# Performance work log

Measured on AMD Instinct MI355X. Metric: run time of the kernel, lower is better.

## Reference

```python
import jax, jax.numpy as jnp
import numpy as np


def setup_inputs() -> dict:
    key = jax.random.key(0)
    k_x, k_qkv, k_proj, k_bias = jax.random.split(key, 4)
    b, n, dim = 4, 8192, 512
    h, w = 8, 256
    x = jax.random.normal(k_x, (b, n, dim), dtype=jnp.float32)
    # Linear weights stored as [in, out] (transpose of torch's [out, in])
    Wqkv = jax.random.normal(k_qkv, (dim, 3 * dim), dtype=jnp.float32) * 0.02
    bqkv = jnp.zeros((3 * dim,), dtype=jnp.float32)
    Wproj = jax.random.normal(k_proj, (dim, dim), dtype=jnp.float32) * 0.02
    bproj = jnp.zeros((dim,), dtype=jnp.float32)
    # torch init is zeros; use small randn so the bias path is exercised
    attn_bias = jax.random.normal(k_bias, (h, w, w), dtype=jnp.float32) * 0.02
    return {"x": x, "Wqkv": Wqkv, "bqkv": bqkv, "Wproj": Wproj,
            "bproj": bproj, "attn_bias": attn_bias}


def reference(x, Wqkv, bqkv, Wproj, bproj, attn_bias):
    b, n, c = x.shape
    h, w, _ = attn_bias.shape
    d = c // h
    nw = n // w  # number of non-overlapping windows (n divisible by w)
    qkv = (x @ Wqkv + bqkv).reshape(b, n, 3, h, d)
    q, k, v = jnp.moveaxis(qkv, 2, 0)  # each [b, n, h, d]

    def to_windows(t):
        # [b, n, h, d] -> [b, h, nw, w, d]
        return t.reshape(b, nw, w, h, d).transpose(0, 3, 1, 2, 4)

    q, k, v = to_windows(q), to_windows(k), to_windows(v)
    scale = d ** -0.5
    # block-local attention: [b, h, nw, w, w]
    attn = jnp.einsum('bhnqd,bhnkd->bhnqk', q, k) * scale + attn_bias[None, :, None]
    attn = jax.nn.softmax(attn, axis=-1)
    out = jnp.einsum('bhnqk,bhnkd->bhnqd', attn, v)
    # [b, h, nw, w, d] -> [b, n, h*d]
    out = out.transpose(0, 2, 3, 1, 4).reshape(b, n, c)
    return out @ Wproj + bproj
```

## Files before the change

### kernel.cpp

```cpp
#include <hip/hip_runtime.h>

typedef unsigned short u16;
typedef unsigned int u32;
typedef __bf16 bf16x8 __attribute__((ext_vector_type(8)));
typedef float f32x4 __attribute__((ext_vector_type(4)));


__device__ __forceinline__ u16 f2bf(float f) {
  u32 u = __builtin_bit_cast(u32, f);
  u32 r = (u + 0x7fffu + ((u >> 16) & 1u)) >> 16;
  return (u16)r;
}
__device__ __forceinline__ u32 pk2(float a, float b) {
  return (u32)f2bf(a) | ((u32)f2bf(b) << 16);
}
__device__ __forceinline__ f32x4 mfma16(bf16x8 a, bf16x8 b, f32x4 c) {
  return __builtin_amdgcn_mfma_f32_16x16x32_bf16(a, b, c, 0, 0, 0);
}
__device__ __forceinline__ void glds16(const void* g, void* l) {
  typedef __attribute__((address_space(1))) void as1_void;
  typedef __attribute__((address_space(3))) void as3_void;
  __builtin_amdgcn_global_load_lds((as1_void*)g, (as3_void*)l, 16, 0, 0);
}


__device__ __forceinline__ void transpose_body(const float* __restrict__ in,
                                               u16* __restrict__ out,
                                               int N, int n0, int k0) {
  __shared__ float t[32][33];
  int tx = threadIdx.x & 31, ty = threadIdx.x >> 5;
#pragma unroll
  for (int s = 0; s < 32; s += 8)
    t[ty + s][tx] = in[(long)(k0 + ty + s) * N + n0 + tx];
  __syncthreads();
#pragma unroll
  for (int s = 0; s < 32; s += 8)
    out[(long)(n0 + ty + s) * 512 + k0 + tx] = f2bf(t[tx][ty + s]);
}

__launch_bounds__(256)
__global__ void prep_k(const float* __restrict__ x, u16* __restrict__ xbf,
                       const float* __restrict__ Wqkv, u16* __restrict__ wqkvT,
                       const float* __restrict__ Wproj, u16* __restrict__ wprojT,
                       const float* __restrict__ bias, float* __restrict__ biasT) {
  const int id = blockIdx.x;
  if (id < 8192) {
    long i = ((long)id * 256 + threadIdx.x) * 8;
    float4 f0 = *(const float4*)(x + i);
    float4 f1 = *(const float4*)(x + i + 4);
    uint4 o;
    o.x = pk2(f0.x, f0.y);
    o.y = pk2(f0.z, f0.w);
    o.z = pk2(f1.x, f1.y);
    o.w = pk2(f1.z, f1.w);
    *(uint4*)(xbf + i) = o;
  } else if (id < 8960) {
    int bx = id - 8192;
    transpose_body(Wqkv, wqkvT, 1536, (bx % 48) * 32, (bx / 48) * 32);
  } else if (id < 9216) {
    int bx = id - 8960;
    transpose_body(Wproj, wprojT, 512, (bx & 15) * 32, (bx >> 4) * 32);
  } else {
    int hb = id - 9216;
    int h = hb >> 4, rt = hb & 15;
    int lane = threadIdx.x & 63;
    int quad = lane >> 4, l15 = lane & 15;
    int jtg = threadIdx.x >> 6;
    const float L = 1.44269504f;
#pragma unroll
    for (int i = 0; i < 4; ++i) {
      int jt = jtg * 4 + i;
      float4 v = *(const float4*)&bias[((long)h * 256 + rt * 16 + l15) * 256 + jt * 16 + quad * 4];
      v.x *= L; v.y *= L; v.z *= L; v.w *= L;
      *(float4*)&biasT[(((long)hb * 16 + jt) * 64 + lane) * 4] = v;
    }
  }
}


template <int EPI>
__device__ __forceinline__ void gemm_body(const u16* __restrict__ A, const u16* __restrict__ Bt,
                                          const float* __restrict__ bias,
                                          u16* __restrict__ oqk, u16* __restrict__ ovt,
                                          float* __restrict__ ofp,
                                          long arow0, long brow0) {
  constexpr int K = 512;
  __shared__ u16 Asm[8192];
  __shared__ u16 Bsm[8192];

  const int tid = threadIdx.x;
  const int wave = tid >> 6, lane = tid & 63;
  const int quad = lane >> 4, l15 = lane & 15;
  const int wm = wave >> 1, wn = wave & 1;
  const int gsw = quad ^ ((l15 >> 1) & 3);

  f32x4 acc[4][4] = {};

  for (int k0 = 0; k0 < K; k0 += 64) {
#pragma unroll
    for (int rd = 0; rd < 4; ++rd) {
      int flat = rd * 256 + tid;
      int c = flat >> 9, row = (flat >> 2) & 127, gp = flat & 3;
      int g = gp ^ ((row >> 1) & 3);
      const long koff = k0 + c * 32 + g * 8;
      glds16(A + (arow0 + row) * K + koff, &Asm[(rd * 256 + wave * 64) * 8]);
      glds16(Bt + (brow0 + row) * K + koff, &Bsm[(rd * 256 + wave * 64) * 8]);
    }
    __syncthreads();
#pragma unroll
    for (int c = 0; c < 2; ++c) {
      bf16x8 af[4], bfr[4];
#pragma unroll
      for (int i = 0; i < 4; ++i)
        af[i] = *(const bf16x8*)&Asm[c * 4096 + (wm * 64 + i * 16 + l15) * 32 + gsw * 8];
#pragma unroll
      for (int j = 0; j < 4; ++j)
        bfr[j] = *(const bf16x8*)&Bsm[c * 4096 + (wn * 64 + j * 16 + l15) * 32 + gsw * 8];
#pragma unroll
      for (int i = 0; i < 4; ++i)
#pragma unroll
        for (int j = 0; j < 4; ++j)
          acc[i][j] = mfma16(af[i], bfr[j], acc[i][j]);
    }
    __syncthreads();
  }

#pragma unroll
  for (int j = 0; j < 4; ++j) {
    const int C = (int)brow0 + wn * 64 + j * 16 + l15;
    const float bc = bias[C];
#pragma unroll
    for (int i = 0; i < 4; ++i) {
      const long R0 = arow0 + wm * 64 + i * 16 + quad * 4;
      float v4[4];
#pragma unroll
      for (int r = 0; r < 4; ++r) v4[r] = acc[i][j][r] + bc;
      if constexpr (EPI == 0) {
        if (C < 1024) {
#pragma unroll
          for (int r = 0; r < 4; ++r) oqk[(R0 + r) * 1024 + C] = f2bf(v4[r]);
        } else {
          const int hc = (C >> 6) & 7, dc = C & 63;
          const int b = (int)(R0 >> 13), n0 = (int)(R0 & 8191);
          uint2 w;
          w.x = pk2(v4[0], v4[1]);
          w.y = pk2(v4[2], v4[3]);
          *(uint2*)&ovt[((long)(b * 8 + hc) * 64 + dc) * 8192 + n0] = w;
        }
      } else {
#pragma unroll
        for (int r = 0; r < 4; ++r) ofp[(R0 + r) * 512 + C] = v4[r];
      }
    }
  }
}


__launch_bounds__(256)
__global__ void qkv_gemm_k(const u16* __restrict__ A, const u16* __restrict__ Bt,
                           const float* __restrict__ bias,
                           u16* __restrict__ oqk, u16* __restrict__ ovt) {
  int bid = blockIdx.x;
  int xcd = bid & 7, i = bid >> 3;
  int nt = i % 12, mtl = i / 12;
  gemm_body<0>(A, Bt, bias, oqk, ovt, nullptr,
               (long)(xcd * 32 + mtl) * 128, (long)nt * 128);
}

__launch_bounds__(256)
__global__ void proj_gemm_k(const u16* __restrict__ A, const u16* __restrict__ Bt,
                            const float* __restrict__ bias, float* __restrict__ ofp) {
  int bid = blockIdx.x;
  int xcd = bid & 7, i = bid >> 3;
  int nt = i & 3, mtl = i >> 2;
  gemm_body<1>(A, Bt, bias, nullptr, nullptr, ofp,
               (long)(xcd * 32 + mtl) * 128, (long)nt * 128);
}


__launch_bounds__(512, 4)
__global__ void attn_win(const u16* __restrict__ qk, const u16* __restrict__ vtb,
                         const float* __restrict__ biasT, u16* __restrict__ og) {
  __shared__ __align__(16) u16 kS[16384];
  __shared__ __align__(16) u16 vS[16384];
  __shared__ __align__(16) u16 pS[8][1024];

  const int tid = threadIdx.x;
  const int wave = tid >> 6, lane = tid & 63;
  const int quad = lane >> 4, l15 = lane & 15;
  const int gsw = quad ^ ((l15 >> 1) & 3);

  const int wi = blockIdx.x;
  const int xcd = wi & 7, hi = (wi >> 3) & 7, wl = wi >> 6;
  const int win = xcd * 16 + wl;
  const int nwi = win & 31, bi = win >> 5;
  const long grow = (long)bi * 8192 + nwi * 256;
  const u16* qp = qk + grow * 1024 + hi * 64;
  const u16* kp = qp + 512;
  const u16* vp = vtb + (long)(bi * 8 + hi) * 64 * 8192 + nwi * 256;

  bf16x8 bq[2][2];
#pragma unroll
  for (int sc = 0; sc < 2; ++sc) {
    const int q0 = wave * 32 + sc * 16;
    bq[sc][0] = *(const bf16x8*)&qp[(long)(q0 + l15) * 1024 + quad * 8];
    bq[sc][1] = *(const bf16x8*)&qp[(long)(q0 + l15) * 1024 + 32 + quad * 8];
  }

#pragma unroll
  for (int it = 0; it < 4; ++it) {
    int flat = it * 512 + tid;
    int t = flat >> 3, dg = flat & 7;
    int c = dg >> 2, gp = (dg & 3) ^ ((t >> 1) & 3);
    int4 val = *(const int4*)&kp[(long)t * 1024 + dg * 8];
    *(int4*)&kS[c * 8192 + t * 32 + gp * 8] = val;
  }
#pragma unroll
  for (int it = 0; it < 4; ++it) {
    int flat = it * 512 + tid;
    int d = flat >> 5, tg = flat & 31;
    int kk = tg >> 2, gp = (tg & 3) ^ ((d >> 1) & 3);
    int4 val = *(const int4*)&vp[(long)d * 8192 + tg * 8];
    *(int4*)&vS[kk * 2048 + d * 32 + gp * 8] = val;
  }
  __syncthreads();

  u16* Pw = pS[wave];
  const float cscale = 0.18033688f;

#pragma unroll
  for (int sc = 0; sc < 2; ++sc) {
    const int q0 = wave * 32 + sc * 16;
    const int rt = wave * 2 + sc;
    const float* bT = &biasT[(long)(hi * 16 + rt) * 16 * 64 * 4];

    f32x4 sum4 = {0.f, 0.f, 0.f, 0.f};
    f32x4 o[4] = {};

#pragma unroll
    for (int m = 0; m < 4; ++m) {
#pragma unroll
      for (int j2 = 0; j2 < 4; ++j2) {
        const int jt = m * 4 + j2;
        bf16x8 a0 = *(const bf16x8*)&kS[(jt * 16 + l15) * 32 + gsw * 8];
        bf16x8 a1 = *(const bf16x8*)&kS[8192 + (jt * 16 + l15) * 32 + gsw * 8];
        f32x4 z = {0.f, 0.f, 0.f, 0.f};
        z = mfma16(a0, bq[sc][0], z);
        z = mfma16(a1, bq[sc][1], z);
        f32x4 bb = *(const f32x4*)&bT[(long)jt * 256 + lane * 4];
        f32x4 p;
#pragma unroll
        for (int r = 0; r < 4; ++r) {
          p[r] = __builtin_exp2f(z[r] * cscale + bb[r]);
          sum4[r] += p[r];
        }
        const int gp = ((jt & 1) * 2 + (quad >> 1)) ^ ((l15 >> 1) & 3);
        const int slot = (jt >> 1) & 1;
        uint2 w;
        w.x = pk2(p[0], p[1]);
        w.y = pk2(p[2], p[3]);
        *(uint2*)&Pw[slot * 512 + l15 * 32 + gp * 8 + (quad & 1) * 4] = w;
      }
#pragma unroll
      for (int kk2 = 0; kk2 < 2; ++kk2) {
        const int kk = m * 2 + kk2;
        bf16x8 bp = *(const bf16x8*)&Pw[kk2 * 512 + l15 * 32 + gsw * 8];
#pragma unroll
        for (int dt = 0; dt < 4; ++dt) {
          bf16x8 av = *(const bf16x8*)&vS[kk * 2048 + (dt * 16 + l15) * 32 + gsw * 8];
          o[dt] = mfma16(av, bp, o[dt]);
        }
      }
    }

    float sum = (sum4[0] + sum4[1]) + (sum4[2] + sum4[3]);
    sum += __shfl_xor(sum, 16);
    sum += __shfl_xor(sum, 32);
    const float inv = 1.0f / sum;

    const long rowoff = (grow + q0 + l15) * 512 + hi * 64 + quad * 4;
#pragma unroll
    for (int dt = 0; dt < 4; ++dt) {
      uint2 w;
      w.x = pk2(o[dt][0] * inv, o[dt][1] * inv);
      w.y = pk2(o[dt][2] * inv, o[dt][3] * inv);
      *(uint2*)&og[rowoff + dt * 16] = w;
    }
  }
}


extern "C" void kernel_launch(void* const* d_in, const int* in_sizes, int n_in,
                              void* d_out, int out_size, void* d_ws, size_t ws_size,
                              hipStream_t stream) {
  const float* x     = (const float*)d_in[0];
  const float* Wqkv  = (const float*)d_in[1];
  const float* bqkv  = (const float*)d_in[2];
  const float* Wproj = (const float*)d_in[3];
  const float* bproj = (const float*)d_in[4];
  const float* abias = (const float*)d_in[5];
  float* out = (float*)d_out;

  char* ws = (char*)d_ws;
  u16*   qkp    = (u16*)(ws);
  u16*   vtb    = (u16*)(ws + 67108864L);
  u16*   wqkvT  = (u16*)(ws + 100663296L);
  u16*   wprojT = (u16*)(ws + 102236160L);
  float* biasTp = (float*)(ws + 102760448L);
  u16*   xbf    = (u16*)(ws + 104857600L);
  u16*   attnout = xbf;

  prep_k<<<9344, 256, 0, stream>>>(x, xbf, Wqkv, wqkvT, Wproj, wprojT, abias, biasTp);
  qkv_gemm_k<<<3072, 256, 0, stream>>>(xbf, wqkvT, bqkv, qkp, vtb);
  attn_win<<<1024, 512, 0, stream>>>(qkp, vtb, biasTp, attnout);
  proj_gemm_k<<<1024, 256, 0, stream>>>(attnout, wprojT, bproj, out);
}
```

Baseline: 279.6 us.

## Use 256x256 double-buffered GEMM tiles with 8 waves and interleaved prefetch

Both GEMMs move from 128x128 tiles with 4 waves and a single LDS buffer to 256x256 tiles with 8 waves and double-buffered LDS. Loads for the next K-slice are issued between MFMA sub-phases, paced by explicit waitcnt and s_barrier, and s_setprio raises priority around MFMA bursts. The aim is to overlap global-to-LDS transfers with compute and raise data reuse per tile. In exchange, LDS use grows to 128KB per block and the grid shrinks (768 and 256 blocks), which may reduce occupancy and leave a tail for the projection GEMM.

```diff
diff --git a/kernel.cpp b/kernel.cpp
--- a/kernel.cpp
+++ b/kernel.cpp
@@ -85,44 +85,123 @@
                                           float* __restrict__ ofp,
                                           long arow0, long brow0) {
   constexpr int K = 512;
-  __shared__ u16 Asm[8192];
-  __shared__ u16 Bsm[8192];
+  constexpr int NT = 8;
+  __shared__ u16 Asm[2][16384];
+  __shared__ u16 Bsm[2][16384];
 
   const int tid = threadIdx.x;
   const int wave = tid >> 6, lane = tid & 63;
   const int quad = lane >> 4, l15 = lane & 15;
-  const int wm = wave >> 1, wn = wave & 1;
+  const int wm = wave >> 2, wn = wave & 3;
   const int gsw = quad ^ ((l15 >> 1) & 3);
 
-  f32x4 acc[4][4] = {};
-
-  for (int k0 = 0; k0 < K; k0 += 64) {
-#pragma unroll
-    for (int rd = 0; rd < 4; ++rd) {
-      int flat = rd * 256 + tid;
-      int c = flat >> 9, row = (flat >> 2) & 127, gp = flat & 3;
-      int g = gp ^ ((row >> 1) & 3);
-      const long koff = k0 + c * 32 + g * 8;
-      glds16(A + (arow0 + row) * K + koff, &Asm[(rd * 256 + wave * 64) * 8]);
-      glds16(Bt + (brow0 + row) * K + koff, &Bsm[(rd * 256 + wave * 64) * 8]);
-    }
-    __syncthreads();
+  const int srow = tid >> 2;
+  const int sg = (tid & 3) ^ ((srow >> 1) & 3);
+
+  auto stA = [&](int buf, int t, int mh) {
+#pragma unroll
+    for (int ld = 0; ld < 2; ++ld)
+      glds16(A + (arow0 + mh * 128 + srow) * K + t * 64 + ld * 32 + sg * 8,
+             &Asm[buf][(ld * 1024 + mh * 512 + wave * 64) * 8]);
+  };
+  auto stB = [&](int buf, int t, int mh) {
+#pragma unroll
+    for (int ld = 0; ld < 2; ++ld)
+      glds16(Bt + (brow0 + mh * 128 + srow) * K + t * 64 + ld * 32 + sg * 8,
+             &Bsm[buf][(ld * 1024 + mh * 512 + wave * 64) * 8]);
+  };
+
+  f32x4 acc[8][4] = {};
+  bf16x8 aA[2][4], b0[2][2], b1[2][2];
+
+  stA(0, 0, 0); stA(0, 0, 1); stB(0, 0, 0); stB(0, 0, 1);
+  stB(1, 1, 0); stB(1, 1, 1);
+  asm volatile("s_waitcnt vmcnt(4)" ::: "memory");
+  __builtin_amdgcn_s_barrier();
+
+#pragma unroll
+  for (int t = 0; t < NT; ++t) {
+    const int buf = t & 1;
+    u16* As = Asm[buf];
+    u16* Bs = Bsm[buf];
+
 #pragma unroll
     for (int c = 0; c < 2; ++c) {
-      bf16x8 af[4], bfr[4];
-#pragma unroll
-      for (int i = 0; i < 4; ++i)
-        af[i] = *(const bf16x8*)&Asm[c * 4096 + (wm * 64 + i * 16 + l15) * 32 + gsw * 8];
-#pragma unroll
-      for (int j = 0; j < 4; ++j)
-        bfr[j] = *(const bf16x8*)&Bsm[c * 4096 + (wn * 64 + j * 16 + l15) * 32 + gsw * 8];
-#pragma unroll
-      for (int i = 0; i < 4; ++i)
-#pragma unroll
-        for (int j = 0; j < 4; ++j)
-          acc[i][j] = mfma16(af[i], bfr[j], acc[i][j]);
-    }
-    __syncthreads();
+#pragma unroll
+      for (int i = 0; i < 4; ++i)
+        aA[c][i] = *(const bf16x8*)&As[(c * 256 + wm * 128 + i * 16 + l15) * 32 + gsw * 8];
+#pragma unroll
+      for (int j = 0; j < 2; ++j)
+        b0[c][j] = *(const bf16x8*)&Bs[(c * 256 + wn * 64 + j * 16 + l15) * 32 + gsw * 8];
+    }
+    if (t + 1 < NT) stA(buf ^ 1, t + 1, 0);
+    __builtin_amdgcn_s_barrier();
+    asm volatile("s_waitcnt lgkmcnt(0)" ::: "memory");
+    __builtin_amdgcn_s_setprio(1);
+#pragma unroll
+    for (int c = 0; c < 2; ++c)
+#pragma unroll
+      for (int i = 0; i < 4; ++i)
+#pragma unroll
+        for (int j = 0; j < 2; ++j)
+          acc[i][j] = mfma16(aA[c][i], b0[c][j], acc[i][j]);
+    __builtin_amdgcn_s_setprio(0);
+    __builtin_amdgcn_s_barrier();
+
+#pragma unroll
+    for (int c = 0; c < 2; ++c)
+#pragma unroll
+      for (int j = 0; j < 2; ++j)
+        b1[c][j] = *(const bf16x8*)&Bs[(c * 256 + wn * 64 + (2 + j) * 16 + l15) * 32 + gsw * 8];
+    if (t + 1 < NT) stA(buf ^ 1, t + 1, 1);
+    __builtin_amdgcn_s_barrier();
+    asm volatile("s_waitcnt lgkmcnt(0)" ::: "memory");
+    __builtin_amdgcn_s_setprio(1);
+#pragma unroll
+    for (int c = 0; c < 2; ++c)
+#pragma unroll
+      for (int i = 0; i < 4; ++i)
+#pragma unroll
+        for (int j = 0; j < 2; ++j)
+          acc[i][2 + j] = mfma16(aA[c][i], b1[c][j], acc[i][2 + j]);
+    __builtin_amdgcn_s_setprio(0);
+    __builtin_amdgcn_s_barrier();
+
+#pragma unroll
+    for (int c = 0; c < 2; ++c)
+#pragma unroll
+      for (int i = 0; i < 4; ++i)
+        aA[c][i] = *(const bf16x8*)&As[(c * 256 + wm * 128 + (4 + i) * 16 + l15) * 32 + gsw * 8];
+    if (t + 2 < NT) stB(buf, t + 2, 0);
+    __builtin_amdgcn_s_barrier();
+    asm volatile("s_waitcnt lgkmcnt(0)" ::: "memory");
+    __builtin_amdgcn_s_setprio(1);
+#pragma unroll
+    for (int c = 0; c < 2; ++c)
+#pragma unroll
+      for (int i = 0; i < 4; ++i)
+#pragma unroll
+        for (int j = 0; j < 2; ++j)
+          acc[4 + i][j] = mfma16(aA[c][i], b0[c][j], acc[4 + i][j]);
+    __builtin_amdgcn_s_setprio(0);
+    __builtin_amdgcn_s_barrier();
+
+    if (t + 2 < NT) stB(buf, t + 2, 1);
+    __builtin_amdgcn_s_barrier();
+    __builtin_amdgcn_s_setprio(1);
+#pragma unroll
+    for (int c = 0; c < 2; ++c)
+#pragma unroll
+      for (int i = 0; i < 4; ++i)
+#pragma unroll
+        for (int j = 0; j < 2; ++j)
+          acc[4 + i][2 + j] = mfma16(aA[c][i], b1[c][j], acc[4 + i][2 + j]);
+    __builtin_amdgcn_s_setprio(0);
+    if (t < NT - 2)
+      asm volatile("s_waitcnt vmcnt(4)" ::: "memory");
+    else if (t == NT - 2)
+      asm volatile("s_waitcnt vmcnt(0)" ::: "memory");
+    if (t < NT - 1) __builtin_amdgcn_s_barrier();
   }
 
 #pragma unroll
@@ -130,8 +209,8 @@
     const int C = (int)brow0 + wn * 64 + j * 16 + l15;
     const float bc = bias[C];
 #pragma unroll
-    for (int i = 0; i < 4; ++i) {
-      const long R0 = arow0 + wm * 64 + i * 16 + quad * 4;
+    for (int i = 0; i < 8; ++i) {
+      const long R0 = arow0 + wm * 128 + i * 16 + quad * 4;
       float v4[4];
 #pragma unroll
       for (int r = 0; r < 4; ++r) v4[r] = acc[i][j][r] + bc;
@@ -156,25 +235,25 @@
 }
 
 
-__launch_bounds__(256)
+__launch_bounds__(512, 2)
 __global__ void qkv_gemm_k(const u16* __restrict__ A, const u16* __restrict__ Bt,
                            const float* __restrict__ bias,
                            u16* __restrict__ oqk, u16* __restrict__ ovt) {
   int bid = blockIdx.x;
   int xcd = bid & 7, i = bid >> 3;
-  int nt = i % 12, mtl = i / 12;
+  int nt = i % 6, mtl = i / 6;
   gemm_body<0>(A, Bt, bias, oqk, ovt, nullptr,
-               (long)(xcd * 32 + mtl) * 128, (long)nt * 128);
-}
-
-__launch_bounds__(256)
+               (long)(xcd * 16 + mtl) * 256, (long)nt * 256);
+}
+
+__launch_bounds__(512, 2)
 __global__ void proj_gemm_k(const u16* __restrict__ A, const u16* __restrict__ Bt,
                             const float* __restrict__ bias, float* __restrict__ ofp) {
   int bid = blockIdx.x;
   int xcd = bid & 7, i = bid >> 3;
-  int nt = i & 3, mtl = i >> 2;
+  int nt = i & 1, mtl = i >> 1;
   gemm_body<1>(A, Bt, bias, nullptr, nullptr, ofp,
-               (long)(xcd * 32 + mtl) * 128, (long)nt * 128);
+               (long)(xcd * 16 + mtl) * 256, (long)nt * 256);
 }
 
 
@@ -311,7 +390,7 @@
   u16*   attnout = xbf;
 
   prep_k<<<9344, 256, 0, stream>>>(x, xbf, Wqkv, wqkvT, Wproj, wprojT, abias, biasTp);
-  qkv_gemm_k<<<3072, 256, 0, stream>>>(xbf, wqkvT, bqkv, qkp, vtb);
+  qkv_gemm_k<<<768, 512, 0, stream>>>(xbf, wqkvT, bqkv, qkp, vtb);
   attn_win<<<1024, 512, 0, stream>>>(qkp, vtb, biasTp, attnout);
-  proj_gemm_k<<<1024, 256, 0, stream>>>(attnout, wprojT, bproj, out);
-}
+  proj_gemm_k<<<256, 512, 0, stream>>>(attnout, wprojT, bproj, out);
+}
```

After: 300.4 us. 7.4% more time.
